# Kernel optimization log

Hardware: AMD Instinct MI355X
Metric: run time of the kernel (lower is better)

Reference implementation:

```python
import jax, jax.numpy as jnp
import numpy as np

B, H, W, MD = 1, 128, 256, 66
LD, NH, HD, S = 64, 8, 8, 16   # learnable_dim, n_heads, head_dim, shared_hidden
KS, J = 21, 25                 # disco basis functions, neighbors per output point
HMLP, FFN_H = 32, 256

def _gelu(x):
    return jax.nn.gelu(x, approximate=False)

def _build_nbr():
    # 5x5 geodesic window: clamp at poles (lat), wrap in longitude
    ii = np.clip(np.arange(H)[:, None] + np.arange(-2, 3)[None, :], 0, H - 1)  # [H,5]
    jj = (np.arange(W)[:, None] + np.arange(-2, 3)[None, :]) % W               # [W,5]
    nbr = ii[:, None, :, None] * W + jj[None, :, None, :]                      # [H,W,5,5]
    return nbr.reshape(H * W, J).astype(np.int32)

def setup_inputs() -> dict:
    key = jax.random.key(0)
    ks = jax.random.split(key, 16)
    x = jax.random.normal(ks[0], (B, H, W, MD), dtype=jnp.float32)
    nbr = jnp.asarray(_build_nbr())
    # sparse DiSCO basis values (nonnegative, piecewise-linear style), weights, bias
    psi = jax.random.uniform(ks[1], (H * W, J, KS), dtype=jnp.float32) / J
    disco_w = jax.random.normal(ks[2], (S, KS), dtype=jnp.float32) * 0.2
    disco_b = jax.random.normal(ks[3], (S,), dtype=jnp.float32) * 0.02
    # LatModulator: 2 -> 2S -> 2S MLP on (sin_lat, cos_lat)
    lm_w1 = jax.random.normal(ks[4], (2, 2 * S), dtype=jnp.float32) * 0.3
    lm_b1 = jnp.zeros((2 * S,), dtype=jnp.float32)
    lm_w2 = jax.random.normal(ks[5], (2 * S, 2 * S), dtype=jnp.float32) * 0.2
    lm_b2 = jnp.concatenate([jnp.ones((S,), jnp.float32), jnp.zeros((S,), jnp.float32)])  # gamma~1, beta~0
    # per-head MLPs: S -> HMLP -> 1, stacked over heads
    h_w1 = jax.random.normal(ks[6], (NH, S, HMLP), dtype=jnp.float32) * (1.0 / np.sqrt(S))
    h_b1 = jnp.zeros((NH, HMLP), dtype=jnp.float32)
    h_w2 = jax.random.normal(ks[7], (NH, HMLP), dtype=jnp.float32) * (1.0 / np.sqrt(HMLP))
    h_b2 = jnp.zeros((NH,), dtype=jnp.float32)
    # FFN: model_dim -> FFN_H -> learnable_dim; last-2 input cols zeroed (init per source)
    f_w1 = jax.random.normal(ks[8], (MD, FFN_H), dtype=jnp.float32) * (1.0 / np.sqrt(MD))
    f_w1 = f_w1.at[-2:, :].set(0.0)
    f_b1 = jnp.zeros((FFN_H,), dtype=jnp.float32)
    f_w2 = jax.random.normal(ks[9], (FFN_H, LD), dtype=jnp.float32) * (1.0 / np.sqrt(FFN_H))
    f_b2 = jnp.zeros((LD,), dtype=jnp.float32)
    return dict(x=x, nbr=nbr, psi=psi, disco_w=disco_w, disco_b=disco_b,
                lm_w1=lm_w1, lm_b1=lm_b1, lm_w2=lm_w2, lm_b2=lm_b2,
                h_w1=h_w1, h_b1=h_b1, h_w2=h_w2, h_b2=h_b2,
                f_w1=f_w1, f_b1=f_b1, f_w2=f_w2, f_b2=f_b2)

def reference(x, nbr, psi, disco_w, disco_b, lm_w1, lm_b1, lm_w2, lm_b2,
              h_w1, h_b1, h_w2, h_b2, f_w1, f_b1, f_w2, f_b2):
    x_learn = x[..., :LD]               # (B,H,W,LD)
    sin_cos = x[..., LD:]               # (B,H,W,2)
    # --- sparse DiSCO conv, 1 input channel per map, shared over all maps ---
    xmaps = x_learn.transpose(0, 3, 1, 2).reshape(B * LD, H * W)   # (BL, P)
    xg = xmaps[:, nbr]                                             # (BL, P, J) irregular gather
    Wp = jnp.einsum('pjk,ok->pjo', psi, disco_w)                   # (P, J, S)
    y = jnp.einsum('npj,pjo->npo', xg, Wp) + disco_b               # (BL, P, S)
    disco_out = y.reshape(B, LD, H, W, S).transpose(0, 2, 3, 1, 4) # (B,H,W,LD,S)
    # --- FiLM latitude modulation ---
    scr = sin_cos[:, :, 0, :]                                      # (B,H,2)
    m = _gelu(scr @ lm_w1 + lm_b1) @ lm_w2 + lm_b2                 # (B,H,2S)
    gamma = m[..., :S][:, :, None, None, :]                        # (B,H,1,1,S)
    beta = m[..., S:][:, :, None, None, :]
    disco_out = disco_out * gamma + beta
    # --- per-head MLPs (S -> HMLP -> 1), vectorized over heads ---
    d5 = disco_out.reshape(B, H, W, NH, HD, S)
    h1 = _gelu(jnp.einsum('bhwnds,nsc->bhwndc', d5, h_w1) + h_b1[:, None, :].reshape(NH, 1, HMLP))
    ho = jnp.einsum('bhwndc,nc->bhwnd', h1, h_w2) + h_b2[None, None, None, :, None]
    x_learn2 = ho.reshape(B, H, W, LD) + x_learn                   # residual
    # --- FFN channel mixing ---
    x_full = jnp.concatenate([x_learn2, sin_cos], axis=-1)
    f = _gelu(x_full @ f_w1 + f_b1) @ f_w2 + f_b2                  # (B,H,W,LD)
    out_learn = f + x_learn2
    return jnp.concatenate([out_learn, sin_cos], axis=-1)
```

## Files before the change

kernel.cpp:

```cpp
#include <hip/hip_runtime.h>
#include <math.h>

#define HDIM 128
#define WDIM 256
#define NPIX (HDIM*WDIM)
#define LD 64
#define S 16
#define J 25
#define KS 21
#define NH 8
#define HMLP 32
#define FFN_H 256
#define PSI_ROW (J*KS)
#define WP_ROW (J*S)

__device__ __forceinline__ float gelu_exact(float v) {
    return 0.5f * v * (1.0f + erff(v * 0.70710678118654752440f));
}

__device__ __forceinline__ float gelu_fast(float x) {
    float x2 = x * x;
    float a  = __builtin_fmaf(x2, 0.035677408136f, 0.7978845608028654f);
    float z  = a * x * 2.885390081777927f;
    z = fmaxf(-30.f, fminf(30.f, z));
    float e  = __builtin_exp2f(z);
    float th = (e - 1.f) * __builtin_amdgcn_rcpf(e + 1.f);
    float s  = 0.5f * x;
    return __builtin_fmaf(s, th, s);
}

__global__ __launch_bounds__(128) void k_mod(
    const float* __restrict__ x, const float* __restrict__ lm_w1,
    const float* __restrict__ lm_b1, const float* __restrict__ lm_w2,
    const float* __restrict__ lm_b2, float* __restrict__ gb)
{
    int h = threadIdx.x;
    float s0 = x[h * WDIM * 66 + 64];
    float s1 = x[h * WDIM * 66 + 65];
    float t[32];
#pragma unroll
    for (int j = 0; j < 32; ++j)
        t[j] = gelu_exact(s0 * lm_w1[j] + s1 * lm_w1[32 + j] + lm_b1[j]);
#pragma unroll
    for (int j = 0; j < 32; ++j) {
        float m = lm_b2[j];
#pragma unroll
        for (int cc = 0; cc < 32; ++cc) m += t[cc] * lm_w2[cc * 32 + j];
        gb[h * 32 + j] = m;
    }
}

__global__ __launch_bounds__(256) void k_wp(
    const float* __restrict__ psi, const float* __restrict__ disco_w,
    float* __restrict__ wp)
{
    __shared__ alignas(16) float psi_s[4][J * 24];
    __shared__ alignas(16) float dw_s[16 * 28];

    const int tid = threadIdx.x;
    const int wid = tid >> 6;
    const int lane = tid & 63;

    for (int i = tid; i < 16 * KS; i += 256) dw_s[(i / KS) * 28 + (i % KS)] = disco_w[i];
    __syncthreads();

    const int p = blockIdx.x * 4 + wid;
    const float* pr = psi + (size_t)p * PSI_ROW;
#pragma unroll
    for (int t = 0; t < 9; ++t) {
        int idx = t * 64 + lane;
        if (idx < PSI_ROW) {
            int j = idx / KS, k = idx - j * KS;
            psi_s[wid][j * 24 + k] = pr[idx];
        }
    }
    asm volatile("s_waitcnt lgkmcnt(0) vmcnt(0)" ::: "memory");

#pragma unroll
    for (int i = 0; i < 7; ++i) {
        int e = i * 64 + lane;
        if (e < WP_ROW) {
            int j = e >> 4, o = e & 15;
            const float* pj = &psi_s[wid][j * 24];
            const float* wo = &dw_s[o * 28];
            float acc = pj[20] * wo[20];
#pragma unroll
            for (int t = 0; t < 5; ++t) {
                float4 a = *(const float4*)(pj + t * 4);
                float4 b = *(const float4*)(wo + t * 4);
                acc += a.x * b.x + a.y * b.y + a.z * b.z + a.w * b.w;
            }
            wp[(size_t)p * WP_ROW + e] = acc;
        }
    }
}

__device__ __forceinline__ float head_mlp(
    const float y[16], int n, const float* __restrict__ hw1_s,
    const float* __restrict__ hb1_s, const float* __restrict__ hw2_s)
{
    float ho = 0.f;
#pragma unroll
    for (int c8 = 0; c8 < 4; ++c8) {
        float t8[8];
        {
            const float4* hb = (const float4*)&hb1_s[n * 36 + c8 * 8];
            float4 b0 = hb[0], b1 = hb[1];
            t8[0] = b0.x; t8[1] = b0.y; t8[2] = b0.z; t8[3] = b0.w;
            t8[4] = b1.x; t8[5] = b1.y; t8[6] = b1.z; t8[7] = b1.w;
        }
#pragma unroll
        for (int s = 0; s < 16; ++s) {
            float ys = y[s];
            const float* hr = &hw1_s[n * 516 + s * 32 + c8 * 8];
            float4 h0 = *(const float4*)(hr);
            float4 h1 = *(const float4*)(hr + 4);
            t8[0] += ys * h0.x; t8[1] += ys * h0.y;
            t8[2] += ys * h0.z; t8[3] += ys * h0.w;
            t8[4] += ys * h1.x; t8[5] += ys * h1.y;
            t8[6] += ys * h1.z; t8[7] += ys * h1.w;
        }
#pragma unroll
        for (int j = 0; j < 8; ++j)
            ho += gelu_fast(t8[j]) * hw2_s[n * 33 + c8 * 8 + j];
    }
    return ho;
}

__global__ __launch_bounds__(256) void k_disco(
    const float* __restrict__ x, const float* __restrict__ wp,
    const float* __restrict__ disco_b, const float* __restrict__ gb,
    const float* __restrict__ h_w1, const float* __restrict__ h_b1,
    const float* __restrict__ h_w2, const float* __restrict__ h_b2,
    float* __restrict__ x2out)
{
    __shared__ alignas(16) float4 wp_s[4][J * 4];
    __shared__ alignas(16) float hw1_s[8 * 516];
    __shared__ alignas(16) float hb1_s[8 * 36];
    __shared__ float hw2_s[8 * 33];
    __shared__ float hb2_s[8];

    const int tid = threadIdx.x;
    const int wid = tid >> 6;
    const int lane = tid & 63;

    for (int i = tid; i < NH * S * HMLP; i += 256) {
        int n = i >> 9;
        hw1_s[n * 516 + (i & 511)] = h_w1[i];
    }
    { int i = tid; hw2_s[(i >> 5) * 33 + (i & 31)] = h_w2[i]; }
    { int i = tid; hb1_s[(i >> 5) * 36 + (i & 31)] = h_b1[i]; }
    if (tid < 8)  hb2_s[tid] = h_b2[tid];
    __syncthreads();

    const int pbase = (blockIdx.x * 4 + wid) * 8;
    const int h = pbase >> 8;
    const int w0 = pbase & 255;
    const int c = lane;
    const int n = lane >> 3;

    int rowoff[5];
#pragma unroll
    for (int a = 0; a < 5; ++a) {
        int hh = h + a - 2;
        hh = hh < 0 ? 0 : (hh > HDIM - 1 ? HDIM - 1 : hh);
        rowoff[a] = hh << 8;
    }

    float gbr[16], ber[16], dbr[16];
    {
        const float* gbp = gb + h * 32;
#pragma unroll
        for (int o4 = 0; o4 < 4; ++o4) {
            float4 g  = *(const float4*)(gbp + o4 * 4);
            float4 be = *(const float4*)(gbp + 16 + o4 * 4);
            float4 d  = *(const float4*)(disco_b + o4 * 4);
            gbr[o4*4+0] = g.x;  gbr[o4*4+1] = g.y;  gbr[o4*4+2] = g.z;  gbr[o4*4+3] = g.w;
            ber[o4*4+0] = be.x; ber[o4*4+1] = be.y; ber[o4*4+2] = be.z; ber[o4*4+3] = be.w;
            dbr[o4*4+0] = d.x;  dbr[o4*4+1] = d.y;  dbr[o4*4+2] = d.z;  dbr[o4*4+3] = d.w;
        }
    }
    const float hb2r = hb2_s[n];

    for (int it = 0; it < 8; ++it) {
        const int p = pbase + it;
        const int w = w0 + it;

        const float4* wpg = (const float4*)(wp + (size_t)p * WP_ROW);
#pragma unroll
        for (int t = 0; t < 2; ++t) {
            int idx = t * 64 + lane;
            if (idx < J * 4) wp_s[wid][idx] = wpg[idx];
        }
        asm volatile("s_waitcnt lgkmcnt(0) vmcnt(0)" ::: "memory");

        float y[16];
#pragma unroll
        for (int o = 0; o < 16; ++o) y[o] = dbr[o];

        float xc = 0.f;
#pragma unroll
        for (int a = 0; a < 5; ++a) {
#pragma unroll
            for (int b = 0; b < 5; ++b) {
                int ww = (w + b - 2) & 255;
                float xv = x[(size_t)(rowoff[a] + ww) * 66 + c];
                if (a == 2 && b == 2) xc = xv;
                const float4* wrow = &wp_s[wid][(a * 5 + b) * 4];
#pragma unroll
                for (int o4 = 0; o4 < 4; ++o4) {
                    float4 wv = wrow[o4];
                    y[o4 * 4 + 0] += xv * wv.x;
                    y[o4 * 4 + 1] += xv * wv.y;
                    y[o4 * 4 + 2] += xv * wv.z;
                    y[o4 * 4 + 3] += xv * wv.w;
                }
            }
        }

#pragma unroll
        for (int o = 0; o < 16; ++o)
            y[o] = y[o] * gbr[o] + ber[o];

        float ho = head_mlp(y, n, hw1_s, hb1_s, hw2_s);

        x2out[(size_t)p * 64 + c] = ho + hb2r + xc;
    }
}

__global__ __launch_bounds__(256) void k_ffn1(
    const float* __restrict__ x2, const float* __restrict__ f_w1,
    const float* __restrict__ f_b1, float* __restrict__ f1t)
{
    __shared__ alignas(16) float rowbuf[4][64];
    __shared__ float ttile[4][64][65];

    const int tid = threadIdx.x;
    const int w   = tid >> 6;
    const int ln  = tid & 63;
    const int p0  = blockIdx.x * 64;

    float wreg[64];
#pragma unroll
    for (int k = 0; k < 64; ++k)
        wreg[k] = f_w1[k * FFN_H + w * 64 + ln];
    const float bias = f_b1[w * 64 + ln];

    for (int px = 0; px < 64; ++px) {
        const int p = p0 + px;
        rowbuf[w][ln] = x2[(size_t)p * 64 + ln];
        asm volatile("s_waitcnt lgkmcnt(0) vmcnt(0)" ::: "memory");

        float acc = bias;
#pragma unroll
        for (int k4 = 0; k4 < 16; ++k4) {
            float4 xv = *(const float4*)&rowbuf[w][k4 * 4];
            acc += xv.x * wreg[k4 * 4 + 0] + xv.y * wreg[k4 * 4 + 1]
                 + xv.z * wreg[k4 * 4 + 2] + xv.w * wreg[k4 * 4 + 3];
        }
        ttile[w][px][ln] = gelu_fast(acc);
    }
    asm volatile("s_waitcnt lgkmcnt(0)" ::: "memory");

    for (int r = 0; r < 64; ++r)
        f1t[(size_t)(w * 64 + r) * NPIX + p0 + ln] = ttile[w][ln][r];
}

__global__ __launch_bounds__(256) void k_ffn2(
    const float* __restrict__ x, const float* __restrict__ x2,
    const float* __restrict__ f1t, const float* __restrict__ f_w2,
    const float* __restrict__ f_b2, float* __restrict__ out)
{
    __shared__ alignas(16) float w2s[256 * 32];

    const int tid = threadIdx.x;
    const int wv  = tid >> 6;
    const int ln  = tid & 63;
    const int half  = blockIdx.x & 1;
    const int cbase = half * 32;
    const int p0    = (blockIdx.x >> 1) * 256;

    for (int i = tid; i < 256 * 32; i += 256)
        w2s[i] = f_w2[(i >> 5) * 64 + cbase + (i & 31)];
    __syncthreads();

    const int p = p0 + wv * 64 + ln;

    float acc[32];
#pragma unroll
    for (int c4 = 0; c4 < 8; ++c4) {
        float4 bv = *(const float4*)(f_b2 + cbase + c4 * 4);
        acc[c4 * 4 + 0] = bv.x; acc[c4 * 4 + 1] = bv.y;
        acc[c4 * 4 + 2] = bv.z; acc[c4 * 4 + 3] = bv.w;
    }

    for (int q = 0; q < FFN_H; ++q) {
        float f1v = f1t[(size_t)q * NPIX + p];
        const float4* wr = (const float4*)&w2s[q * 32];
#pragma unroll
        for (int c4 = 0; c4 < 8; ++c4) {
            float4 wv = wr[c4];
            acc[c4 * 4 + 0] += f1v * wv.x;
            acc[c4 * 4 + 1] += f1v * wv.y;
            acc[c4 * 4 + 2] += f1v * wv.z;
            acc[c4 * 4 + 3] += f1v * wv.w;
        }
    }

    const float4* x2p = (const float4*)(x2 + (size_t)p * 64 + cbase);
#pragma unroll
    for (int c4 = 0; c4 < 8; ++c4) {
        float4 xv = x2p[c4];
        out[(size_t)p * 66 + cbase + c4 * 4 + 0] = acc[c4 * 4 + 0] + xv.x;
        out[(size_t)p * 66 + cbase + c4 * 4 + 1] = acc[c4 * 4 + 1] + xv.y;
        out[(size_t)p * 66 + cbase + c4 * 4 + 2] = acc[c4 * 4 + 2] + xv.z;
        out[(size_t)p * 66 + cbase + c4 * 4 + 3] = acc[c4 * 4 + 3] + xv.w;
    }
    if (half) {
        out[(size_t)p * 66 + 64] = x[(size_t)p * 66 + 64];
        out[(size_t)p * 66 + 65] = x[(size_t)p * 66 + 65];
    }
}

extern "C" void kernel_launch(void* const* d_in, const int* in_sizes, int n_in,
                              void* d_out, int out_size, void* d_ws, size_t ws_size,
                              hipStream_t stream) {
    const float* x       = (const float*)d_in[0];
    const float* psi     = (const float*)d_in[2];
    const float* disco_w = (const float*)d_in[3];
    const float* disco_b = (const float*)d_in[4];
    const float* lm_w1   = (const float*)d_in[5];
    const float* lm_b1   = (const float*)d_in[6];
    const float* lm_w2   = (const float*)d_in[7];
    const float* lm_b2   = (const float*)d_in[8];
    const float* h_w1    = (const float*)d_in[9];
    const float* h_b1    = (const float*)d_in[10];
    const float* h_w2    = (const float*)d_in[11];
    const float* h_b2    = (const float*)d_in[12];
    const float* f_w1    = (const float*)d_in[13];
    const float* f_b1    = (const float*)d_in[14];
    const float* f_w2    = (const float*)d_in[15];
    const float* f_b2    = (const float*)d_in[16];
    float* out = (float*)d_out;

    float* gb  = (float*)d_ws;
    float* x2  = gb + 4096;
    float* wp  = x2 + (size_t)NPIX * 64;
    float* f1t = wp;

    k_mod  <<<1,    128, 0, stream>>>(x, lm_w1, lm_b1, lm_w2, lm_b2, gb);
    k_wp   <<<8192, 256, 0, stream>>>(psi, disco_w, wp);
    k_disco<<<1024, 256, 0, stream>>>(x, wp, disco_b, gb,
                                      h_w1, h_b1, h_w2, h_b2, x2);
    k_ffn1 <<<512,  256, 0, stream>>>(x2, f_w1, f_b1, f1t);
    k_ffn2 <<<256,  256, 0, stream>>>(x, x2, f1t, f_w2, f_b2, out);
}
```

Measured before the change: 440.3 us.

## Register-cache disco weights, halve disco work per wave, prefetch FFN1 rows

```diff
diff --git a/kernel.cpp b/kernel.cpp
--- a/kernel.cpp
+++ b/kernel.cpp
@@ -64,6 +64,20 @@
     for (int i = tid; i < 16 * KS; i += 256) dw_s[(i / KS) * 28 + (i % KS)] = disco_w[i];
     __syncthreads();
 
+    const int o  = lane & 15;
+    const int jg = lane >> 4;
+    float dwr[21];
+    {
+        const float* wo = &dw_s[o * 28];
+#pragma unroll
+        for (int t = 0; t < 5; ++t) {
+            float4 v = *(const float4*)(wo + t * 4);
+            dwr[t * 4 + 0] = v.x; dwr[t * 4 + 1] = v.y;
+            dwr[t * 4 + 2] = v.z; dwr[t * 4 + 3] = v.w;
+        }
+        dwr[20] = wo[20];
+    }
+
     const int p = blockIdx.x * 4 + wid;
     const float* pr = psi + (size_t)p * PSI_ROW;
 #pragma unroll
@@ -78,19 +92,17 @@
 
 #pragma unroll
     for (int i = 0; i < 7; ++i) {
-        int e = i * 64 + lane;
-        if (e < WP_ROW) {
-            int j = e >> 4, o = e & 15;
+        int j = jg + 4 * i;
+        if (j < J) {
             const float* pj = &psi_s[wid][j * 24];
-            const float* wo = &dw_s[o * 28];
-            float acc = pj[20] * wo[20];
+            float acc = pj[20] * dwr[20];
 #pragma unroll
             for (int t = 0; t < 5; ++t) {
                 float4 a = *(const float4*)(pj + t * 4);
-                float4 b = *(const float4*)(wo + t * 4);
-                acc += a.x * b.x + a.y * b.y + a.z * b.z + a.w * b.w;
+                acc += a.x * dwr[t * 4 + 0] + a.y * dwr[t * 4 + 1]
+                     + a.z * dwr[t * 4 + 2] + a.w * dwr[t * 4 + 3];
             }
-            wp[(size_t)p * WP_ROW + e] = acc;
+            wp[(size_t)p * WP_ROW + j * 16 + o] = acc;
         }
     }
 }
@@ -138,6 +150,7 @@
     __shared__ alignas(16) float hw1_s[8 * 516];
     __shared__ alignas(16) float hb1_s[8 * 36];
     __shared__ float hw2_s[8 * 33];
+    __shared__ alignas(16) float db_s[16];
     __shared__ float hb2_s[8];
 
     const int tid = threadIdx.x;
@@ -150,10 +163,11 @@
     }
     { int i = tid; hw2_s[(i >> 5) * 33 + (i & 31)] = h_w2[i]; }
     { int i = tid; hb1_s[(i >> 5) * 36 + (i & 31)] = h_b1[i]; }
+    if (tid < 16) db_s[tid] = disco_b[tid];
     if (tid < 8)  hb2_s[tid] = h_b2[tid];
     __syncthreads();
 
-    const int pbase = (blockIdx.x * 4 + wid) * 8;
+    const int pbase = (blockIdx.x * 4 + wid) * 4;
     const int h = pbase >> 8;
     const int w0 = pbase & 255;
     const int c = lane;
@@ -166,23 +180,9 @@
         hh = hh < 0 ? 0 : (hh > HDIM - 1 ? HDIM - 1 : hh);
         rowoff[a] = hh << 8;
     }
-
-    float gbr[16], ber[16], dbr[16];
-    {
-        const float* gbp = gb + h * 32;
-#pragma unroll
-        for (int o4 = 0; o4 < 4; ++o4) {
-            float4 g  = *(const float4*)(gbp + o4 * 4);
-            float4 be = *(const float4*)(gbp + 16 + o4 * 4);
-            float4 d  = *(const float4*)(disco_b + o4 * 4);
-            gbr[o4*4+0] = g.x;  gbr[o4*4+1] = g.y;  gbr[o4*4+2] = g.z;  gbr[o4*4+3] = g.w;
-            ber[o4*4+0] = be.x; ber[o4*4+1] = be.y; ber[o4*4+2] = be.z; ber[o4*4+3] = be.w;
-            dbr[o4*4+0] = d.x;  dbr[o4*4+1] = d.y;  dbr[o4*4+2] = d.z;  dbr[o4*4+3] = d.w;
-        }
-    }
-    const float hb2r = hb2_s[n];
-
-    for (int it = 0; it < 8; ++it) {
+    const float* gbp = gb + h * 32;
+
+    for (int it = 0; it < 4; ++it) {
         const int p = pbase + it;
         const int w = w0 + it;
 
@@ -196,7 +196,11 @@
 
         float y[16];
 #pragma unroll
-        for (int o = 0; o < 16; ++o) y[o] = dbr[o];
+        for (int o4 = 0; o4 < 4; ++o4) {
+            float4 d = ((const float4*)db_s)[o4];
+            y[o4 * 4 + 0] = d.x; y[o4 * 4 + 1] = d.y;
+            y[o4 * 4 + 2] = d.z; y[o4 * 4 + 3] = d.w;
+        }
 
         float xc = 0.f;
 #pragma unroll
@@ -220,11 +224,11 @@
 
 #pragma unroll
         for (int o = 0; o < 16; ++o)
-            y[o] = y[o] * gbr[o] + ber[o];
+            y[o] = y[o] * gbp[o] + gbp[16 + o];
 
         float ho = head_mlp(y, n, hw1_s, hb1_s, hw2_s);
 
-        x2out[(size_t)p * 64 + c] = ho + hb2r + xc;
+        x2out[(size_t)p * 64 + c] = ho + hb2_s[n] + xc;
     }
 }
 
@@ -246,10 +250,13 @@
         wreg[k] = f_w1[k * FFN_H + w * 64 + ln];
     const float bias = f_b1[w * 64 + ln];
 
+    float cur = x2[(size_t)p0 * 64 + ln];
     for (int px = 0; px < 64; ++px) {
-        const int p = p0 + px;
-        rowbuf[w][ln] = x2[(size_t)p * 64 + ln];
-        asm volatile("s_waitcnt lgkmcnt(0) vmcnt(0)" ::: "memory");
+        float nxtv = 0.f;
+        if (px < 63) nxtv = x2[(size_t)(p0 + px + 1) * 64 + ln];
+
+        rowbuf[w][ln] = cur;
+        asm volatile("s_waitcnt lgkmcnt(0)" ::: "memory");
 
         float acc = bias;
 #pragma unroll
@@ -259,6 +266,7 @@
                  + xv.z * wreg[k4 * 4 + 2] + xv.w * wreg[k4 * 4 + 3];
         }
         ttile[w][px][ln] = gelu_fast(acc);
+        cur = nxtv;
     }
     asm volatile("s_waitcnt lgkmcnt(0)" ::: "memory");
 
@@ -350,7 +358,7 @@
 
     k_mod  <<<1,    128, 0, stream>>>(x, lm_w1, lm_b1, lm_w2, lm_b2, gb);
     k_wp   <<<8192, 256, 0, stream>>>(psi, disco_w, wp);
-    k_disco<<<1024, 256, 0, stream>>>(x, wp, disco_b, gb,
+    k_disco<<<2048, 256, 0, stream>>>(x, wp, disco_b, gb,
                                       h_w1, h_b1, h_w2, h_b2, x2);
     k_ffn1 <<<512,  256, 0, stream>>>(x2, f_w1, f_b1, f1t);
     k_ffn2 <<<256,  256, 0, stream>>>(x, x2, f1t, f_w2, f_b2, out);
```

Measured after the change: 362.7 us. 17.6% less time.
